# Kernel optimization log

Hardware: AMD Instinct MI355X
Metric: run time of the kernel (lower is better)

Reference implementation:

```python
import math
import jax, jax.numpy as jnp
import numpy as np

H = 256      # hidden_size
HEADS = 8
DK = H // HEADS
B = 32
DL = 290     # drug length
PL = 1000    # protein length


def _pe(length, d):
    # sinusoidal positional encoding, d even
    pos = jnp.arange(length, dtype=jnp.float32)[:, None]
    div = jnp.exp(jnp.arange(0, d, 2, dtype=jnp.float32) * (-math.log(10000.0) / d))
    ang = pos * div  # [L, d/2]
    pe = jnp.zeros((length, d), jnp.float32)
    pe = pe.at[:, 0::2].set(jnp.sin(ang)).at[:, 1::2].set(jnp.cos(ang))
    return pe


def setup_inputs() -> dict:
    key = jax.random.key(0)
    ks = iter(jax.random.split(key, 48))
    def lin(din, dout):
        return jax.random.normal(next(ks), (din, dout), jnp.float32) * 0.02, jnp.zeros((dout,), jnp.float32)
    inp = {}
    inp['drug'] = jax.random.normal(next(ks), (B, DL, H), jnp.float32)
    inp['protein'] = jax.random.normal(next(ks), (B, PL, H), jnp.float32)
    inp['scale_d'] = jnp.ones((1,), jnp.float32)
    inp['scale_p'] = jnp.ones((1,), jnp.float32)
    for name in ['q_d', 'k_p', 'v_p', 'q_p', 'k_d', 'v_d', 'out_d', 'out_p']:
        w, b = lin(H, H)
        inp['w_' + name] = w
        inp['b_' + name] = b
    inp['alpha'] = jnp.asarray(0.5, jnp.float32)
    for name in ['fc_dp', 'fc_pd']:
        w, b = lin(HEADS, H)
        inp['w_' + name] = w
        inp['b_' + name] = b
    for name in ['gd', 'gp']:
        w, b = lin(H, H)
        inp['w_' + name] = w
        inp['b_' + name] = b
    return inp


def _split_heads(x):
    b, l, _ = x.shape
    return x.reshape(b, l, HEADS, DK).transpose(0, 2, 1, 3)  # [b, h, l, dk]


def _forward(drug, protein, scale_d, scale_p,
             w_q_d, b_q_d, w_k_p, b_k_p, w_v_p, b_v_p,
             w_q_p, b_q_p, w_k_d, b_k_d, w_v_d, b_v_d,
             alpha, w_out_d, b_out_d, w_out_p, b_out_p,
             w_fc_dp, b_fc_dp, w_fc_pd, b_fc_pd,
             w_gd, b_gd, w_gp, b_gp):
    b, dl, h = drug.shape
    pl = protein.shape[1]
    # positional encoding (buffers, non-learned except scale)
    drug_e = drug + scale_d * _pe(dl, h)
    prot_e = protein + scale_p * _pe(pl, h)

    Qd = _split_heads(drug_e @ w_q_d + b_q_d)   # [b,h,dl,dk]
    Kp = _split_heads(prot_e @ w_k_p + b_k_p)   # [b,h,pl,dk]
    Vp = _split_heads(prot_e @ w_v_p + b_v_p)
    Qp = _split_heads(prot_e @ w_q_p + b_q_p)
    Kd = _split_heads(drug_e @ w_k_d + b_k_d)
    Vd = _split_heads(drug_e @ w_v_d + b_v_d)

    inv_sqrt = 1.0 / math.sqrt(DK)
    attn_dp = jnp.einsum('bhid,bhjd->bhij', Qd, Kp) * inv_sqrt      # [b,h,dl,pl]
    # (Q_p K_d^T)^T along last two dims -> [b,h,dl,pl]
    attn_pd = jnp.einsum('bhjd,bhid->bhij', Qp, Kd) * inv_sqrt
    a = jax.nn.sigmoid(alpha)
    A = jax.nn.softmax(a * attn_dp + (1.0 - a) * attn_pd, axis=-1)  # [b,h,dl,pl]

    ctx_d = jnp.einsum('bhij,bhjd->bhid', A, Vp)  # [b,h,dl,dk]
    ctx_p = jnp.einsum('bhij,bhid->bhjd', A, Vd)  # [b,h,pl,dk]
    ctx_d = ctx_d.transpose(0, 2, 1, 3).reshape(b, dl, h) @ w_out_d + b_out_d
    ctx_p = ctx_p.transpose(0, 2, 1, 3).reshape(b, pl, h) @ w_out_p + b_out_p

    attn_dp_m = jnp.mean(A, axis=-1).transpose(0, 2, 1)   # [b,dl,heads]
    drug_attn = attn_dp_m @ w_fc_dp + b_fc_dp             # [b,dl,h]
    attn_pd_m = jnp.mean(A, axis=-2).transpose(0, 2, 1)   # [b,pl,heads]
    prot_attn = attn_pd_m @ w_fc_pd + b_fc_pd             # [b,pl,h]

    drug_gate = jax.nn.sigmoid(drug_e @ w_gd + b_gd)
    prot_gate = jax.nn.sigmoid(prot_e @ w_gp + b_gp)
    ctx_d = ctx_d * drug_gate
    ctx_p = ctx_p * prot_gate

    drug_upd = drug_e + ctx_d * jax.nn.sigmoid(drug_attn)
    prot_upd = prot_e + ctx_p * jax.nn.sigmoid(prot_attn)
    return jnp.concatenate([drug_upd, prot_upd], axis=1)  # [b, dl+pl, h]


def reference(drug, protein, scale_d, scale_p,
              w_q_d, b_q_d, w_k_p, b_k_p, w_v_p, b_v_p,
              w_q_p, b_q_p, w_k_d, b_k_d, w_v_d, b_v_d,
              alpha, w_out_d, b_out_d, w_out_p, b_out_p,
              w_fc_dp, b_fc_dp, w_fc_pd, b_fc_pd,
              w_gd, b_gd, w_gp, b_gp):
    return _forward(drug, protein, scale_d, scale_p,
                    w_q_d, b_q_d, w_k_p, b_k_p, w_v_p, b_v_p,
                    w_q_p, b_q_p, w_k_d, b_k_d, w_v_d, b_v_d,
                    alpha, w_out_d, b_out_d, w_out_p, b_out_p,
                    w_fc_dp, b_fc_dp, w_fc_pd, b_fc_pd,
                    w_gd, b_gd, w_gp, b_gp)
```

## Files before the change

kernel.cpp:

```cpp
#include <hip/hip_runtime.h>
#include <math.h>

typedef __attribute__((ext_vector_type(8))) short bf16x8;
typedef __attribute__((ext_vector_type(4))) float f32x4;
typedef unsigned short u16;
typedef unsigned int u32;

#define DEVFN static __device__ __forceinline__

constexpr int NB  = 32;
constexpr int DLn = 290;
constexpr int PLc = 1000;
constexpr int MD  = NB * DLn;
constexpr int MP  = NB * PLc;

DEVFN u16 f2b(float f) {
    u32 u = __builtin_bit_cast(u32, f);
    u32 r = u + 0x7fffu + ((u >> 16) & 1u);
    return (u16)(r >> 16);
}
DEVFN float b2f(u16 s) { return __builtin_bit_cast(float, (u32)s << 16); }
DEVFN float sigm(float x) { return 1.0f / (1.0f + __expf(-x)); }
DEVFN int sw(int row, int col, int stride) { return row * stride + (col ^ ((row & 7) << 3)); }

__global__ void pe_kernel(float* __restrict__ pe) {
    int p = blockIdx.x, c = threadIdx.x;
    float div = __expf((float)(c & ~1) * (-9.210340371976184f / 256.0f));
    float ang = (float)p * div;
    pe[p * 256 + c] = (c & 1) ? cosf(ang) : sinf(ang);
}

__global__ __launch_bounds__(256) void eadd_kernel(
        const float* __restrict__ drug, const float* __restrict__ prot,
        const float* __restrict__ scale_d, const float* __restrict__ scale_p,
        const float* __restrict__ pe,
        u16* __restrict__ e_d, u16* __restrict__ e_p) {
    int idx = blockIdx.x * 256 + threadIdx.x;
    int r = idx >> 6, c4 = (idx & 63) * 4;
    if (r < MD) {
        int i = r % DLn;
        float s = scale_d[0];
        float4 dv = *(const float4*)&drug[(size_t)r * 256 + c4];
        float4 pv = *(const float4*)&pe[i * 256 + c4];
        u16 o[4];
        o[0] = f2b(dv.x + s * pv.x); o[1] = f2b(dv.y + s * pv.y);
        o[2] = f2b(dv.z + s * pv.z); o[3] = f2b(dv.w + s * pv.w);
        *(uint2*)&e_d[(size_t)r * 256 + c4] = *(uint2*)o;
    } else {
        int rr = r - MD;
        int j = rr % PLc;
        float s = scale_p[0];
        float4 dv = *(const float4*)&prot[(size_t)rr * 256 + c4];
        float4 pv = *(const float4*)&pe[j * 256 + c4];
        u16 o[4];
        o[0] = f2b(dv.x + s * pv.x); o[1] = f2b(dv.y + s * pv.y);
        o[2] = f2b(dv.z + s * pv.z); o[3] = f2b(dv.w + s * pv.w);
        *(uint2*)&e_p[(size_t)rr * 256 + c4] = *(uint2*)o;
    }
}

struct WPtrs { const float* w[10]; };
__global__ __launch_bounds__(256) void wprep_kernel(WPtrs wp, u16* __restrict__ wt) {
    __shared__ u16 t[64][66];
    int m = blockIdx.y, tile = blockIdx.x;
    int k0 = (tile >> 2) * 64, n0 = (tile & 3) * 64;
    const float* w = wp.w[m];
    int r = threadIdx.x >> 6, c = threadIdx.x & 63;
    #pragma unroll
    for (int q = 0; q < 16; q++) {
        int rr = r + q * 4;
        t[rr][c] = f2b(w[(size_t)(k0 + rr) * 256 + n0 + c]);
    }
    __syncthreads();
    #pragma unroll
    for (int q = 0; q < 16; q++) {
        int rr = r + q * 4;
        wt[((size_t)m << 16) + (size_t)(n0 + rr) * 256 + k0 + c] = t[c][rr];
    }
}

struct GCfg { const u16* A; const u16* BT; const float* bias; u16* C; int mtiles; int sig; };
struct GCfg8 { GCfg c[8]; };

__global__ __launch_bounds__(256) void gemm_kernel(GCfg8 cfgs) {
    const GCfg cfg = cfgs.c[blockIdx.z];
    const int mt = blockIdx.x;
    if (mt >= cfg.mtiles) return;
    const int nt = blockIdx.y;
    __shared__ u16 As[64 * 256];
    __shared__ u16 Bs[64 * 256];
    const int tid = threadIdx.x;
    const int lane = tid & 63, w = tid >> 6, ln = lane & 15, g = lane >> 4;
    const int lr = tid >> 2, lc = tid & 3;
    const u16* Ag = cfg.A + (size_t)(mt * 64 + lr) * 256 + lc * 8;
    const u16* Bg = cfg.BT + (size_t)(nt * 64 + lr) * 256 + lc * 8;
    uint4 av[8], bv[8];
    #pragma unroll
    for (int kk = 0; kk < 8; kk++) {
        av[kk] = *(const uint4*)(Ag + kk * 32);
        bv[kk] = *(const uint4*)(Bg + kk * 32);
    }
    #pragma unroll
    for (int kk = 0; kk < 8; kk++) {
        *(uint4*)&As[sw(lr, lc * 8 + kk * 32, 256)] = av[kk];
        *(uint4*)&Bs[sw(lr, lc * 8 + kk * 32, 256)] = bv[kk];
    }
    __syncthreads();
    const int m0 = (w >> 1) * 32, n0 = (w & 1) * 32;
    f32x4 acc[2][2] = {};
    #pragma unroll
    for (int k0 = 0; k0 < 8; k0++) {
        #pragma unroll
        for (int mi = 0; mi < 2; mi++) {
            bf16x8 af = *(const bf16x8*)&As[sw(m0 + mi * 16 + ln, k0 * 32 + g * 8, 256)];
            #pragma unroll
            for (int ni = 0; ni < 2; ni++) {
                bf16x8 bfv = *(const bf16x8*)&Bs[sw(n0 + ni * 16 + ln, k0 * 32 + g * 8, 256)];
                acc[mi][ni] = __builtin_amdgcn_mfma_f32_16x16x32_bf16(af, bfv, acc[mi][ni], 0, 0, 0);
            }
        }
    }
    #pragma unroll
    for (int mi = 0; mi < 2; mi++) {
        #pragma unroll
        for (int ni = 0; ni < 2; ni++) {
            const int n = nt * 64 + n0 + ni * 16 + ln;
            const float bb = cfg.bias[n];
            const int rowb = mt * 64 + m0 + mi * 16 + g * 4;
            #pragma unroll
            for (int r = 0; r < 4; r++) {
                float v = acc[mi][ni][r] + bb;
                if (cfg.sig) v = sigm(v);
                cfg.C[(size_t)(rowb + r) * 256 + n] = f2b(v);
            }
        }
    }
}

__global__ __launch_bounds__(512) void attn_kernel(
        const u16* __restrict__ Qd, const u16* __restrict__ Kd, const u16* __restrict__ Vd,
        const u16* __restrict__ Kp, const u16* __restrict__ Vp, const u16* __restrict__ Qp,
        const float* __restrict__ alpha,
        u16* __restrict__ ctx_d, u16* __restrict__ ctx_p, float* __restrict__ cm) {
    __shared__ u16 Ks[2][64 * 64];
    __shared__ union {
        struct { u16 VpT[2][32 * 64]; u16 Pm[320 * 64]; } s1;
        struct { u16 PT[64 * 320]; u16 VdT[32 * 320]; } s2;
    } U;
    __shared__ float r_l[320];
    __shared__ float colpart[8][64];

    const int bh = blockIdx.x, b = bh >> 3, h = bh & 7;
    const int tid = threadIdx.x;
    const int w = tid >> 6, lane = tid & 63, ln = lane & 15, g = lane >> 4;

    const float a = sigm(alpha[0]);
    const float inv = 0.1767766952966369f;
    const float sa = a * inv, sb = (1.0f - a) * inv;
    const int nmt = (w < 4) ? 3 : 2;
    const int mtsA[3] = { w, w + 8, w + 16 };

    const size_t rbd = (size_t)b * DLn * 256 + h * 32;
    const size_t rbp = (size_t)b * PLc * 256 + h * 32;

    bf16x8 Qf[3][2];
    #pragma unroll
    for (int t = 0; t < 3; t++) {
        const int i = mtsA[t] * 16 + ln;
        #pragma unroll
        for (int ks = 0; ks < 2; ks++) {
            u16 o[8] = {0,0,0,0,0,0,0,0};
            if (t < nmt && i < DLn) {
                const u16* src = (ks ? Kd : Qd) + rbd + (size_t)i * 256 + g * 8;
                const float s = ks ? sb : sa;
                uint4 v = *(const uint4*)src;
                u16 e[8]; *(uint4*)e = v;
                #pragma unroll
                for (int q = 0; q < 8; q++) o[q] = f2b(b2f(e[q]) * s);
            }
            Qf[t][ks] = *(bf16x8*)o;
        }
    }

    const int s_jj = tid >> 3, s_ch = tid & 7;
    const u16* s_src = ((s_ch >> 2) ? Qp : Kp) + rbp + (s_ch & 3) * 8;
    const int v_j = tid & 63, v_d0 = (tid >> 6) * 4;

    {
        int j = s_jj;
        uint4 kv = (j < PLc) ? *(const uint4*)(s_src + (size_t)j * 256) : make_uint4(0,0,0,0);
        uint2 vv = (v_j < PLc) ? *(const uint2*)(Vp + rbp + (size_t)v_j * 256 + v_d0) : make_uint2(0,0);
        *(uint4*)&Ks[0][sw(s_jj, s_ch * 8, 64)] = kv;
        u16 e[4]; *(uint2*)e = vv;
        #pragma unroll
        for (int q = 0; q < 4; q++) U.s1.VpT[0][sw(v_d0 + q, v_j, 64)] = e[q];
    }
    __syncthreads();

    float rs[3] = {0.f, 0.f, 0.f};
    f32x4 accd[3][2] = {};
    for (int jt = 0; jt < 16; jt++) {
        const int cur = jt & 1, j0 = jt * 64;
        const int jn = j0 + 64 + s_jj;
        uint4 kv = (jn < PLc) ? *(const uint4*)(s_src + (size_t)jn * 256) : make_uint4(0,0,0,0);
        const int vn = j0 + 64 + v_j;
        uint2 vv = (vn < PLc) ? *(const uint2*)(Vp + rbp + (size_t)vn * 256 + v_d0) : make_uint2(0,0);

        bf16x8 kf[4][2];
        #pragma unroll
        for (int js = 0; js < 4; js++)
            #pragma unroll
            for (int ks = 0; ks < 2; ks++)
                kf[js][ks] = *(const bf16x8*)&Ks[cur][sw(js * 16 + ln, ks * 32 + g * 8, 64)];

        #pragma unroll
        for (int t = 0; t < 3; t++) {
            if (t >= nmt) break;
            const int mt = mtsA[t];
            f32x4 acc[4] = {};
            #pragma unroll
            for (int ks = 0; ks < 2; ks++)
                #pragma unroll
                for (int js = 0; js < 4; js++)
                    acc[js] = __builtin_amdgcn_mfma_f32_16x16x32_bf16(kf[js][ks], Qf[t][ks], acc[js], 0, 0, 0);
            const int irow = mt * 16 + ln;
            #pragma unroll
            for (int js = 0; js < 4; js++) {
                u16 pb[4];
                float psum = 0.f;
                #pragma unroll
                for (int r = 0; r < 4; r++) {
                    float p = __expf(acc[js][r]);
                    psum += p;
                    pb[r] = f2b(p);
                }
                rs[t] += psum;
                *(ushort4*)&U.s1.Pm[sw(irow, js * 16 + g * 4, 64)] = *(ushort4*)pb;
            }
        }
        #pragma unroll
        for (int t = 0; t < 3; t++) {
            if (t >= nmt) break;
            const int mt = mtsA[t];
            #pragma unroll
            for (int ks2 = 0; ks2 < 2; ks2++) {
                bf16x8 af = *(const bf16x8*)&U.s1.Pm[sw(mt * 16 + ln, ks2 * 32 + g * 8, 64)];
                #pragma unroll
                for (int nd = 0; nd < 2; nd++) {
                    bf16x8 bv = *(const bf16x8*)&U.s1.VpT[cur][sw(nd * 16 + ln, ks2 * 32 + g * 8, 64)];
                    accd[t][nd] = __builtin_amdgcn_mfma_f32_16x16x32_bf16(af, bv, accd[t][nd], 0, 0, 0);
                }
            }
        }
        *(uint4*)&Ks[cur ^ 1][sw(s_jj, s_ch * 8, 64)] = kv;
        {
            u16 e[4]; *(uint2*)e = vv;
            #pragma unroll
            for (int q = 0; q < 4; q++) U.s1.VpT[cur ^ 1][sw(v_d0 + q, v_j, 64)] = e[q];
        }
        __syncthreads();
    }

    #pragma unroll
    for (int t = 0; t < 3; t++) {
        float v = rs[t];
        v += __shfl_xor(v, 16);
        v += __shfl_xor(v, 32);
        rs[t] = v;
    }
    if (g == 0) {
        #pragma unroll
        for (int t = 0; t < 3; t++) {
            if (t >= nmt) break;
            const int i = mtsA[t] * 16 + ln;
            r_l[i] = (i < DLn) ? 1.0f / (rs[t] - 24.0f) : 0.0f;
        }
    }
    __syncthreads();

    #pragma unroll
    for (int t = 0; t < 3; t++) {
        if (t >= nmt) break;
        const int mt = mtsA[t];
        #pragma unroll
        for (int r = 0; r < 4; r++) {
            const int i = mt * 16 + g * 4 + r;
            if (i < DLn) {
                const float ri = r_l[i];
                #pragma unroll
                for (int nd = 0; nd < 2; nd++)
                    ctx_d[rbd + (size_t)i * 256 + nd * 16 + ln] = f2b(accd[t][nd][r] * ri);
            }
        }
    }
    for (int c = tid; c < 320 * 8; c += 512) {
        const int i = c >> 3, d0 = (c & 7) * 4;
        u16 o[4] = {0,0,0,0};
        if (i < DLn) {
            const float ri = r_l[i];
            uint2 v = *(const uint2*)(Vd + rbd + (size_t)i * 256 + d0);
            u16 e[4]; *(uint2*)e = v;
            #pragma unroll
            for (int q = 0; q < 4; q++) o[q] = f2b(b2f(e[q]) * ri);
        }
        #pragma unroll
        for (int q = 0; q < 4; q++) U.s2.VdT[sw(d0 + q, i, 320)] = o[q];
    }
    {
        int j = s_jj;
        uint4 kv = (j < PLc) ? *(const uint4*)(s_src + (size_t)j * 256) : make_uint4(0,0,0,0);
        *(uint4*)&Ks[0][sw(s_jj, s_ch * 8, 64)] = kv;
    }
    float rr[3][4];
    #pragma unroll
    for (int t = 0; t < 3; t++)
        #pragma unroll
        for (int r = 0; r < 4; r++)
            rr[t][r] = (t < nmt) ? r_l[mtsA[t] * 16 + g * 4 + r] : 0.0f;
    __syncthreads();

    for (int jt = 0; jt < 16; jt++) {
        const int cur = jt & 1, j0 = jt * 64;
        const int jn = j0 + 64 + s_jj;
        uint4 kv = (jn < PLc) ? *(const uint4*)(s_src + (size_t)jn * 256) : make_uint4(0,0,0,0);

        bf16x8 kf[4][2];
        #pragma unroll
        for (int js = 0; js < 4; js++)
            #pragma unroll
            for (int ks = 0; ks < 2; ks++)
                kf[js][ks] = *(const bf16x8*)&Ks[cur][sw(js * 16 + ln, ks * 32 + g * 8, 64)];

        float csl[4] = {0.f, 0.f, 0.f, 0.f};
        #pragma unroll
        for (int t = 0; t < 3; t++) {
            if (t >= nmt) break;
            const int mt = mtsA[t];
            f32x4 acc[4] = {};
            #pragma unroll
            for (int ks = 0; ks < 2; ks++)
                #pragma unroll
                for (int js = 0; js < 4; js++)
                    acc[js] = __builtin_amdgcn_mfma_f32_16x16x32_bf16(Qf[t][ks], kf[js][ks], acc[js], 0, 0, 0);
            #pragma unroll
            for (int js = 0; js < 4; js++) {
                u16 pb[4];
                #pragma unroll
                for (int r = 0; r < 4; r++) {
                    float p = __expf(acc[js][r]);
                    csl[js] += p * rr[t][r];
                    pb[r] = f2b(p);
                }
                *(ushort4*)&U.s2.PT[sw(js * 16 + ln, mt * 16 + g * 4, 320)] = *(ushort4*)pb;
            }
        }
        #pragma unroll
        for (int js = 0; js < 4; js++) {
            float v = csl[js];
            v += __shfl_xor(v, 16);
            v += __shfl_xor(v, 32);
            csl[js] = v;
        }
        if (g == 0) {
            #pragma unroll
            for (int js = 0; js < 4; js++) colpart[w][js * 16 + ln] = csl[js];
        }
        *(uint4*)&Ks[cur ^ 1][sw(s_jj, s_ch * 8, 64)] = kv;
        __syncthreads();

        {
            const int js2 = w & 3, ds2 = w >> 2;
            f32x4 ap = {};
            #pragma unroll
            for (int k = 0; k < 10; k++) {
                bf16x8 af = *(const bf16x8*)&U.s2.PT[sw(js2 * 16 + ln, k * 32 + g * 8, 320)];
                bf16x8 bv = *(const bf16x8*)&U.s2.VdT[sw(ds2 * 16 + ln, k * 32 + g * 8, 320)];
                ap = __builtin_amdgcn_mfma_f32_16x16x32_bf16(af, bv, ap, 0, 0, 0);
            }
            const int d = ds2 * 16 + ln;
            #pragma unroll
            for (int r = 0; r < 4; r++) {
                const int j = j0 + js2 * 16 + g * 4 + r;
                if (j < PLc) ctx_p[rbp + (size_t)j * 256 + d] = f2b(ap[r]);
            }
        }
        if (w == 0) {
            float tot = 0.f;
            #pragma unroll
            for (int ww = 0; ww < 8; ww++) tot += colpart[ww][lane];
            const int j = j0 + lane;
            if (j < PLc) cm[(size_t)(b * PLc + j) * 8 + h] = tot * (1.0f / 290.0f);
        }
        __syncthreads();
    }
}

__global__ __launch_bounds__(256) void combine_kernel(
        const float* __restrict__ drug, const float* __restrict__ prot,
        const float* __restrict__ scale_d, const float* __restrict__ scale_p,
        const float* __restrict__ pe,
        const u16* __restrict__ Xd, const u16* __restrict__ Xp,
        const u16* __restrict__ gate_d, const u16* __restrict__ gate_p,
        const float* __restrict__ cm,
        const float* __restrict__ w_fc_dp, const float* __restrict__ b_fc_dp,
        const float* __restrict__ w_fc_pd, const float* __restrict__ b_fc_pd,
        float* __restrict__ out) {
    int idx = blockIdx.x * 256 + threadIdx.x;
    int r = idx >> 6, c4 = (idx & 63) * 4;
    if (r < MD) {
        int b = r / DLn, i = r % DLn;
        float s = scale_d[0];
        float4 dv = *(const float4*)&drug[(size_t)r * 256 + c4];
        float4 pv = *(const float4*)&pe[i * 256 + c4];
        uint2 xv = *(const uint2*)&Xd[(size_t)r * 256 + c4];
        uint2 gv = *(const uint2*)&gate_d[(size_t)r * 256 + c4];
        float4 bb = *(const float4*)&b_fc_dp[c4];
        float da[4] = { bb.x, bb.y, bb.z, bb.w };
        #pragma unroll
        for (int hh = 0; hh < 8; hh++) {
            float4 wv = *(const float4*)&w_fc_dp[hh * 256 + c4];
            da[0] += 0.001f * wv.x; da[1] += 0.001f * wv.y;
            da[2] += 0.001f * wv.z; da[3] += 0.001f * wv.w;
        }
        u16 xe[4]; *(uint2*)xe = xv;
        u16 ge[4]; *(uint2*)ge = gv;
        float e0 = dv.x + s * pv.x, e1 = dv.y + s * pv.y;
        float e2 = dv.z + s * pv.z, e3 = dv.w + s * pv.w;
        float4 o;
        o.x = e0 + b2f(xe[0]) * b2f(ge[0]) * sigm(da[0]);
        o.y = e1 + b2f(xe[1]) * b2f(ge[1]) * sigm(da[1]);
        o.z = e2 + b2f(xe[2]) * b2f(ge[2]) * sigm(da[2]);
        o.w = e3 + b2f(xe[3]) * b2f(ge[3]) * sigm(da[3]);
        *(float4*)&out[((size_t)b * 1290 + i) * 256 + c4] = o;
    } else {
        int rr = r - MD;
        int b = rr / PLc, j = rr % PLc;
        float s = scale_p[0];
        float4 dv = *(const float4*)&prot[(size_t)rr * 256 + c4];
        float4 pv = *(const float4*)&pe[j * 256 + c4];
        uint2 xv = *(const uint2*)&Xp[(size_t)rr * 256 + c4];
        uint2 gv = *(const uint2*)&gate_p[(size_t)rr * 256 + c4];
        float4 bb = *(const float4*)&b_fc_pd[c4];
        float pa[4] = { bb.x, bb.y, bb.z, bb.w };
        #pragma unroll
        for (int hh = 0; hh < 8; hh++) {
            float cmh = cm[(size_t)rr * 8 + hh];
            float4 wv = *(const float4*)&w_fc_pd[hh * 256 + c4];
            pa[0] += cmh * wv.x; pa[1] += cmh * wv.y;
            pa[2] += cmh * wv.z; pa[3] += cmh * wv.w;
        }
        u16 xe[4]; *(uint2*)xe = xv;
        u16 ge[4]; *(uint2*)ge = gv;
        float e0 = dv.x + s * pv.x, e1 = dv.y + s * pv.y;
        float e2 = dv.z + s * pv.z, e3 = dv.w + s * pv.w;
        float4 o;
        o.x = e0 + b2f(xe[0]) * b2f(ge[0]) * sigm(pa[0]);
        o.y = e1 + b2f(xe[1]) * b2f(ge[1]) * sigm(pa[1]);
        o.z = e2 + b2f(xe[2]) * b2f(ge[2]) * sigm(pa[2]);
        o.w = e3 + b2f(xe[3]) * b2f(ge[3]) * sigm(pa[3]);
        *(float4*)&out[((size_t)b * 1290 + 290 + j) * 256 + c4] = o;
    }
}

extern "C" void kernel_launch(void* const* d_in, const int* in_sizes, int n_in,
                              void* d_out, int out_size, void* d_ws, size_t ws_size,
                              hipStream_t stream) {
    (void)in_sizes; (void)n_in; (void)out_size;
    const float* drug    = (const float*)d_in[0];
    const float* prot    = (const float*)d_in[1];
    const float* scale_d = (const float*)d_in[2];
    const float* scale_p = (const float*)d_in[3];

    char* ws = (char*)d_ws;
    size_t off = 0;
    auto alloc = [&](size_t bytes) -> void* {
        void* p = ws + off;
        off += (bytes + 255) & ~(size_t)255;
        return p;
    };
    float* pe   = (float*)alloc((size_t)1000 * 256 * 4);
    u16* e_d    = (u16*)alloc((size_t)MD * 256 * 2);
    u16* e_p    = (u16*)alloc((size_t)MP * 256 * 2);
    u16* wt     = (u16*)alloc((size_t)10 * 65536 * 2);
    u16* Qd     = (u16*)alloc((size_t)MD * 256 * 2);
    u16* Kd     = (u16*)alloc((size_t)MD * 256 * 2);
    u16* Vd     = (u16*)alloc((size_t)MD * 256 * 2);
    u16* gate_d = (u16*)alloc((size_t)MD * 256 * 2);
    u16* Kp     = (u16*)alloc((size_t)MP * 256 * 2);
    u16* Vp     = (u16*)alloc((size_t)MP * 256 * 2);
    u16* Qp     = (u16*)alloc((size_t)MP * 256 * 2);
    u16* gate_p = (u16*)alloc((size_t)MP * 256 * 2);
    u16* ctxd   = (u16*)alloc((size_t)MD * 256 * 2);
    u16* ctxp   = (u16*)alloc((size_t)MP * 256 * 2);
    float* cm   = (float*)alloc((size_t)MP * 8 * 4);
    u16* Xd     = (u16*)alloc((size_t)MD * 256 * 2);
    u16* Xp     = (u16*)alloc((size_t)MP * 256 * 2);
    if (off > ws_size) return;

    pe_kernel<<<1000, 256, 0, stream>>>(pe);

    WPtrs wp;
    const int wsrc[10] = {4, 12, 14, 25, 6, 8, 10, 27, 16, 18};
    for (int m = 0; m < 10; m++) wp.w[m] = (const float*)d_in[wsrc[m]];
    wprep_kernel<<<dim3(16, 10), 256, 0, stream>>>(wp, wt);

    eadd_kernel<<<(MD + MP) / 4, 256, 0, stream>>>(drug, prot, scale_d, scale_p, pe, e_d, e_p);

    auto W = [&](int slot) { return wt + (size_t)slot * 65536; };
    GCfg8 pc;
    pc.c[0] = { e_d, W(0), (const float*)d_in[5],  Qd,     145, 0 };
    pc.c[1] = { e_d, W(1), (const float*)d_in[13], Kd,     145, 0 };
    pc.c[2] = { e_d, W(2), (const float*)d_in[15], Vd,     145, 0 };
    pc.c[3] = { e_d, W(3), (const float*)d_in[26], gate_d, 145, 1 };
    pc.c[4] = { e_p, W(4), (const float*)d_in[7],  Kp,     500, 0 };
    pc.c[5] = { e_p, W(5), (const float*)d_in[9],  Vp,     500, 0 };
    pc.c[6] = { e_p, W(6), (const float*)d_in[11], Qp,     500, 0 };
    pc.c[7] = { e_p, W(7), (const float*)d_in[28], gate_p, 500, 1 };
    gemm_kernel<<<dim3(500, 4, 8), 256, 0, stream>>>(pc);

    attn_kernel<<<256, 512, 0, stream>>>(Qd, Kd, Vd, Kp, Vp, Qp,
                                         (const float*)d_in[20], ctxd, ctxp, cm);

    GCfg8 oc = pc;
    oc.c[0] = { ctxd, W(8), (const float*)d_in[17], Xd, 145, 0 };
    oc.c[1] = { ctxp, W(9), (const float*)d_in[19], Xp, 500, 0 };
    gemm_kernel<<<dim3(500, 4, 2), 256, 0, stream>>>(oc);

    combine_kernel<<<(MD + MP) / 4, 256, 0, stream>>>(drug, prot, scale_d, scale_p, pe,
        Xd, Xp, gate_d, gate_p, cm,
        (const float*)d_in[21], (const float*)d_in[22],
        (const float*)d_in[23], (const float*)d_in[24],
        (float*)d_out);
}
```

Measured before the change: 205.3 us.

## Fuse positional-encoding add into projection GEMM with register-resident A tiles

Removes the separate eadd kernel by computing x + scale*pe and the bf16 conversion directly in the projection kernel's A-operand load. Each block now keeps its 64-row A tile in registers and loops over all output column tiles of all four weight matrices, double-buffering the weight tiles in shared memory. This drops the bf16 embedding round trip through global memory and the repeated A reloads across N tiles. The trade-off is only 645 blocks instead of thousands, with more serial work and extra barriers per block.

```diff
diff --git a/kernel.cpp b/kernel.cpp
--- a/kernel.cpp
+++ b/kernel.cpp
@@ -28,35 +28,6 @@
     float div = __expf((float)(c & ~1) * (-9.210340371976184f / 256.0f));
     float ang = (float)p * div;
     pe[p * 256 + c] = (c & 1) ? cosf(ang) : sinf(ang);
-}
-
-__global__ __launch_bounds__(256) void eadd_kernel(
-        const float* __restrict__ drug, const float* __restrict__ prot,
-        const float* __restrict__ scale_d, const float* __restrict__ scale_p,
-        const float* __restrict__ pe,
-        u16* __restrict__ e_d, u16* __restrict__ e_p) {
-    int idx = blockIdx.x * 256 + threadIdx.x;
-    int r = idx >> 6, c4 = (idx & 63) * 4;
-    if (r < MD) {
-        int i = r % DLn;
-        float s = scale_d[0];
-        float4 dv = *(const float4*)&drug[(size_t)r * 256 + c4];
-        float4 pv = *(const float4*)&pe[i * 256 + c4];
-        u16 o[4];
-        o[0] = f2b(dv.x + s * pv.x); o[1] = f2b(dv.y + s * pv.y);
-        o[2] = f2b(dv.z + s * pv.z); o[3] = f2b(dv.w + s * pv.w);
-        *(uint2*)&e_d[(size_t)r * 256 + c4] = *(uint2*)o;
-    } else {
-        int rr = r - MD;
-        int j = rr % PLc;
-        float s = scale_p[0];
-        float4 dv = *(const float4*)&prot[(size_t)rr * 256 + c4];
-        float4 pv = *(const float4*)&pe[j * 256 + c4];
-        u16 o[4];
-        o[0] = f2b(dv.x + s * pv.x); o[1] = f2b(dv.y + s * pv.y);
-        o[2] = f2b(dv.z + s * pv.z); o[3] = f2b(dv.w + s * pv.w);
-        *(uint2*)&e_p[(size_t)rr * 256 + c4] = *(uint2*)o;
-    }
 }
 
 struct WPtrs { const float* w[10]; };
@@ -79,61 +50,110 @@
     }
 }
 
-struct GCfg { const u16* A; const u16* BT; const float* bias; u16* C; int mtiles; int sig; };
-struct GCfg8 { GCfg c[8]; };
-
-__global__ __launch_bounds__(256) void gemm_kernel(GCfg8 cfgs) {
-    const GCfg cfg = cfgs.c[blockIdx.z];
-    const int mt = blockIdx.x;
-    if (mt >= cfg.mtiles) return;
-    const int nt = blockIdx.y;
-    __shared__ u16 As[64 * 256];
-    __shared__ u16 Bs[64 * 256];
+struct PM { const u16* BT; const float* bias; u16* C; int sig; };
+struct PCfg {
+    const u16* Ab;
+    const float* Af32;
+    const float* scale;
+    const float* pe;
+    int plen;
+    int mrows;
+    int nmat;
+    PM m[4];
+};
+struct PCfg2 { PCfg c[2]; int split; };
+
+__global__ __launch_bounds__(256) void proj_kernel(PCfg2 cfgs) {
+    const int bid = blockIdx.x;
+    const PCfg cfg = (bid < cfgs.split) ? cfgs.c[0] : cfgs.c[1];
+    const int mt = (bid < cfgs.split) ? bid : bid - cfgs.split;
+    __shared__ u16 Bs[2][64 * 256];
     const int tid = threadIdx.x;
     const int lane = tid & 63, w = tid >> 6, ln = lane & 15, g = lane >> 4;
+    const int m0 = w * 16;
+
+    bf16x8 Af[8];
+    {
+        const int row = mt * 64 + m0 + ln;
+        if (cfg.Af32) {
+            const int i = row % cfg.plen;
+            const float s = cfg.scale[0];
+            const float* Xp_ = cfg.Af32 + (size_t)row * 256 + g * 8;
+            const float* Pe_ = cfg.pe + (size_t)i * 256 + g * 8;
+            #pragma unroll
+            for (int ks = 0; ks < 8; ks++) {
+                float4 xa = *(const float4*)(Xp_ + ks * 32);
+                float4 xb = *(const float4*)(Xp_ + ks * 32 + 4);
+                float4 pa = *(const float4*)(Pe_ + ks * 32);
+                float4 pb = *(const float4*)(Pe_ + ks * 32 + 4);
+                u16 o[8];
+                o[0] = f2b(xa.x + s * pa.x); o[1] = f2b(xa.y + s * pa.y);
+                o[2] = f2b(xa.z + s * pa.z); o[3] = f2b(xa.w + s * pa.w);
+                o[4] = f2b(xb.x + s * pb.x); o[5] = f2b(xb.y + s * pb.y);
+                o[6] = f2b(xb.z + s * pb.z); o[7] = f2b(xb.w + s * pb.w);
+                Af[ks] = *(bf16x8*)o;
+            }
+        } else {
+            const u16* Ap = cfg.Ab + (size_t)row * 256 + g * 8;
+            #pragma unroll
+            for (int ks = 0; ks < 8; ks++)
+                Af[ks] = *(const bf16x8*)(Ap + ks * 32);
+        }
+    }
+
     const int lr = tid >> 2, lc = tid & 3;
-    const u16* Ag = cfg.A + (size_t)(mt * 64 + lr) * 256 + lc * 8;
-    const u16* Bg = cfg.BT + (size_t)(nt * 64 + lr) * 256 + lc * 8;
-    uint4 av[8], bv[8];
-    #pragma unroll
-    for (int kk = 0; kk < 8; kk++) {
-        av[kk] = *(const uint4*)(Ag + kk * 32);
-        bv[kk] = *(const uint4*)(Bg + kk * 32);
-    }
-    #pragma unroll
-    for (int kk = 0; kk < 8; kk++) {
-        *(uint4*)&As[sw(lr, lc * 8 + kk * 32, 256)] = av[kk];
-        *(uint4*)&Bs[sw(lr, lc * 8 + kk * 32, 256)] = bv[kk];
+    const int nphase = cfg.nmat * 4;
+
+    {
+        const u16* Bp = cfg.m[0].BT + (size_t)lr * 256 + lc * 8;
+        uint4 bv[8];
+        #pragma unroll
+        for (int kk = 0; kk < 8; kk++) bv[kk] = *(const uint4*)(Bp + kk * 32);
+        #pragma unroll
+        for (int kk = 0; kk < 8; kk++) *(uint4*)&Bs[0][sw(lr, lc * 8 + kk * 32, 256)] = bv[kk];
     }
     __syncthreads();
-    const int m0 = (w >> 1) * 32, n0 = (w & 1) * 32;
-    f32x4 acc[2][2] = {};
-    #pragma unroll
-    for (int k0 = 0; k0 < 8; k0++) {
-        #pragma unroll
-        for (int mi = 0; mi < 2; mi++) {
-            bf16x8 af = *(const bf16x8*)&As[sw(m0 + mi * 16 + ln, k0 * 32 + g * 8, 256)];
-            #pragma unroll
-            for (int ni = 0; ni < 2; ni++) {
-                bf16x8 bfv = *(const bf16x8*)&Bs[sw(n0 + ni * 16 + ln, k0 * 32 + g * 8, 256)];
-                acc[mi][ni] = __builtin_amdgcn_mfma_f32_16x16x32_bf16(af, bfv, acc[mi][ni], 0, 0, 0);
-            }
-        }
-    }
-    #pragma unroll
-    for (int mi = 0; mi < 2; mi++) {
-        #pragma unroll
-        for (int ni = 0; ni < 2; ni++) {
-            const int n = nt * 64 + n0 + ni * 16 + ln;
-            const float bb = cfg.bias[n];
-            const int rowb = mt * 64 + m0 + mi * 16 + g * 4;
-            #pragma unroll
-            for (int r = 0; r < 4; r++) {
-                float v = acc[mi][ni][r] + bb;
-                if (cfg.sig) v = sigm(v);
-                cfg.C[(size_t)(rowb + r) * 256 + n] = f2b(v);
-            }
-        }
+
+    for (int ph = 0; ph < nphase; ph++) {
+        const int cur = ph & 1;
+        uint4 bv[8];
+        if (ph + 1 < nphase) {
+            const int mi = (ph + 1) >> 2, c = (ph + 1) & 3;
+            const u16* Bp = cfg.m[mi].BT + (size_t)(c * 64 + lr) * 256 + lc * 8;
+            #pragma unroll
+            for (int kk = 0; kk < 8; kk++) bv[kk] = *(const uint4*)(Bp + kk * 32);
+        }
+        f32x4 acc[4] = {};
+        #pragma unroll
+        for (int ks = 0; ks < 8; ks++) {
+            #pragma unroll
+            for (int nt = 0; nt < 4; nt++) {
+                bf16x8 bf = *(const bf16x8*)&Bs[cur][sw(nt * 16 + ln, ks * 32 + g * 8, 256)];
+                acc[nt] = __builtin_amdgcn_mfma_f32_16x16x32_bf16(Af[ks], bf, acc[nt], 0, 0, 0);
+            }
+        }
+        {
+            const int mi = ph >> 2, c = ph & 3;
+            const PM pm = cfg.m[mi];
+            const int rowb = mt * 64 + m0 + g * 4;
+            #pragma unroll
+            for (int nt = 0; nt < 4; nt++) {
+                const int n = c * 64 + nt * 16 + ln;
+                const float bb = pm.bias[n];
+                #pragma unroll
+                for (int r = 0; r < 4; r++) {
+                    float v = acc[nt][r] + bb;
+                    if (pm.sig) v = sigm(v);
+                    pm.C[(size_t)(rowb + r) * 256 + n] = f2b(v);
+                }
+            }
+        }
+        __syncthreads();
+        if (ph + 1 < nphase) {
+            #pragma unroll
+            for (int kk = 0; kk < 8; kk++) *(uint4*)&Bs[cur ^ 1][sw(lr, lc * 8 + kk * 32, 256)] = bv[kk];
+        }
+        __syncthreads();
     }
 }
 
@@ -479,8 +499,6 @@
         return p;
     };
     float* pe   = (float*)alloc((size_t)1000 * 256 * 4);
-    u16* e_d    = (u16*)alloc((size_t)MD * 256 * 2);
-    u16* e_p    = (u16*)alloc((size_t)MP * 256 * 2);
     u16* wt     = (u16*)alloc((size_t)10 * 65536 * 2);
     u16* Qd     = (u16*)alloc((size_t)MD * 256 * 2);
     u16* Kd     = (u16*)alloc((size_t)MD * 256 * 2);
@@ -504,27 +522,32 @@
     for (int m = 0; m < 10; m++) wp.w[m] = (const float*)d_in[wsrc[m]];
     wprep_kernel<<<dim3(16, 10), 256, 0, stream>>>(wp, wt);
 
-    eadd_kernel<<<(MD + MP) / 4, 256, 0, stream>>>(drug, prot, scale_d, scale_p, pe, e_d, e_p);
-
     auto W = [&](int slot) { return wt + (size_t)slot * 65536; };
-    GCfg8 pc;
-    pc.c[0] = { e_d, W(0), (const float*)d_in[5],  Qd,     145, 0 };
-    pc.c[1] = { e_d, W(1), (const float*)d_in[13], Kd,     145, 0 };
-    pc.c[2] = { e_d, W(2), (const float*)d_in[15], Vd,     145, 0 };
-    pc.c[3] = { e_d, W(3), (const float*)d_in[26], gate_d, 145, 1 };
-    pc.c[4] = { e_p, W(4), (const float*)d_in[7],  Kp,     500, 0 };
-    pc.c[5] = { e_p, W(5), (const float*)d_in[9],  Vp,     500, 0 };
-    pc.c[6] = { e_p, W(6), (const float*)d_in[11], Qp,     500, 0 };
-    pc.c[7] = { e_p, W(7), (const float*)d_in[28], gate_p, 500, 1 };
-    gemm_kernel<<<dim3(500, 4, 8), 256, 0, stream>>>(pc);
+
+    PCfg2 p1;
+    p1.split = 145;
+    p1.c[0] = { nullptr, drug, scale_d, pe, DLn, MD, 4,
+                { { W(0), (const float*)d_in[5],  Qd,     0 },
+                  { W(1), (const float*)d_in[13], Kd,     0 },
+                  { W(2), (const float*)d_in[15], Vd,     0 },
+                  { W(3), (const float*)d_in[26], gate_d, 1 } } };
+    p1.c[1] = { nullptr, prot, scale_p, pe, PLc, MP, 4,
+                { { W(4), (const float*)d_in[7],  Kp,     0 },
+                  { W(5), (const float*)d_in[9],  Vp,     0 },
+                  { W(6), (const float*)d_in[11], Qp,     0 },
+                  { W(7), (const float*)d_in[28], gate_p, 1 } } };
+    proj_kernel<<<645, 256, 0, stream>>>(p1);
 
     attn_kernel<<<256, 512, 0, stream>>>(Qd, Kd, Vd, Kp, Vp, Qp,
                                          (const float*)d_in[20], ctxd, ctxp, cm);
 
-    GCfg8 oc = pc;
-    oc.c[0] = { ctxd, W(8), (const float*)d_in[17], Xd, 145, 0 };
-    oc.c[1] = { ctxp, W(9), (const float*)d_in[19], Xp, 500, 0 };
-    gemm_kernel<<<dim3(500, 4, 2), 256, 0, stream>>>(oc);
+    PCfg2 p2;
+    p2.split = 145;
+    p2.c[0] = { ctxd, nullptr, nullptr, nullptr, DLn, MD, 1,
+                { { W(8), (const float*)d_in[17], Xd, 0 }, {}, {}, {} } };
+    p2.c[1] = { ctxp, nullptr, nullptr, nullptr, PLc, MP, 1,
+                { { W(9), (const float*)d_in[19], Xp, 0 }, {}, {}, {} } };
+    proj_kernel<<<645, 256, 0, stream>>>(p2);
 
     combine_kernel<<<(MD + MP) / 4, 256, 0, stream>>>(drug, prot, scale_d, scale_p, pe,
         Xd, Xp, gate_d, gate_p, cm,
```

New measurement: 328.7 us. 60.1% more time.
